# Performance work log

Measured on AMD Instinct MI355X. Metric: run time of the kernel, lower is better.

## Reference

```python
import jax, jax.numpy as jnp
import numpy as np

LAYERS = 2
HIDDEN = 512
FFN = 2048
HEADS = 8
IMG = (32, 64)
SLEN = IMG[0] * IMG[1]
BSZ = 2
KEY_DIM = HIDDEN // HEADS      # 64
V_DIM = HIDDEN * 2             # 1024
HEAD_SIZE = V_DIM // HEADS     # 128
SCALE_BASE = 512.0
SCALING = KEY_DIM ** (-0.5)
LN_EPS = 1e-5


def xpos_apply(x):
    # x: [..., L, d]  (XPOS rotary with length-dependent decay, downscale=False)
    L, d = x.shape[-2], x.shape[-1]
    half = d // 2
    base = (jnp.arange(0, d, 2, dtype=jnp.float32) + 0.4 * d) / (1.4 * d)  # [half]
    min_pos = -(L // 2)
    pos = jnp.arange(min_pos, L + min_pos, dtype=jnp.float32)              # [L]
    scale = base[None, :] ** (pos[:, None] / SCALE_BASE)                   # [L, half]
    inv_freq = 1.0 / (10000.0 ** (jnp.arange(half, dtype=jnp.float32) / half))
    sinusoid = jnp.arange(L, dtype=jnp.float32)[:, None] * inv_freq[None, :]  # [L, half]
    sin = jnp.repeat(jnp.sin(sinusoid) * scale, 2, axis=-1)                # [L, d]
    cos = jnp.repeat(jnp.cos(sinusoid) * scale, 2, axis=-1)                # [L, d]
    x1 = x[..., 0::2]
    x2 = x[..., 1::2]
    rot = jnp.stack([-x2, x1], axis=-1).reshape(x.shape)  # rotate_every_two
    return x * cos + rot * sin


def layer_norm(x, g, b):
    mu = jnp.mean(x, axis=-1, keepdims=True)
    var = jnp.mean(jnp.square(x - mu), axis=-1, keepdims=True)
    return (x - mu) * jax.lax.rsqrt(var + LN_EPS) * g + b


def attention(x, Wq, Wk, Wv, Wo):
    B, S, _ = x.shape
    q = (x @ Wq).reshape(B, S, HEADS, KEY_DIM).transpose(0, 2, 1, 3)   # [B,H,S,dk]
    k = (x @ Wk).reshape(B, S, HEADS, KEY_DIM).transpose(0, 2, 1, 3)
    v = (x @ Wv).reshape(B, S, HEADS, HEAD_SIZE).transpose(0, 2, 1, 3)  # [B,H,S,hs]
    q = xpos_apply(q)
    k = xpos_apply(k)
    scores = jnp.einsum('bhqd,bhkd->bhqk', q, k)
    att = jax.nn.softmax(scores.astype(jnp.float32), axis=-1).astype(scores.dtype)
    att = att * SCALING  # note: scaling applied AFTER softmax, as in the source
    out = jnp.einsum('bhqk,bhkv->bhqv', att, v)                          # [B,H,S,hs]
    out = out.transpose(0, 2, 1, 3).reshape(B, S, V_DIM)
    return out @ Wo


def setup_inputs() -> dict:
    key = jax.random.key(0)
    ks = jax.random.split(key, 8)
    p = lambda k, shp: jax.random.normal(k, shp, dtype=jnp.float32) * 0.02
    return {
        'x':  jax.random.normal(ks[0], (BSZ, SLEN, HIDDEN), dtype=jnp.float32),
        'Wq': p(ks[1], (LAYERS, HIDDEN, HIDDEN)),
        'Wk': p(ks[2], (LAYERS, HIDDEN, HIDDEN)),
        'Wv': p(ks[3], (LAYERS, HIDDEN, V_DIM)),
        'Wo': p(ks[4], (LAYERS, V_DIM, HIDDEN)),
        'W1': p(ks[5], (LAYERS, HIDDEN, FFN)),
        'b1': jnp.zeros((LAYERS, FFN), jnp.float32),
        'W2': p(ks[6], (LAYERS, FFN, HIDDEN)),
        'b2': jnp.zeros((LAYERS, HIDDEN), jnp.float32),
        'g1': jnp.ones((LAYERS, HIDDEN), jnp.float32),
        'be1': jnp.zeros((LAYERS, HIDDEN), jnp.float32),
        'g2': jnp.ones((LAYERS, HIDDEN), jnp.float32),
        'be2': jnp.zeros((LAYERS, HIDDEN), jnp.float32),
    }


def reference(x, Wq, Wk, Wv, Wo, W1, b1, W2, b2, g1, be1, g2, be2):
    for i in range(LAYERS):
        y = layer_norm(x + attention(x, Wq[i], Wk[i], Wv[i], Wo[i]), g1[i], be1[i])
        ffn = jax.nn.relu(y @ W1[i] + b1[i]) @ W2[i] + b2[i]
        x = layer_norm(y + ffn, g2[i], be2[i])
    return x.reshape(x.shape[0], IMG[0], IMG[1], x.shape[2])
```

## Files before the change

### kernel.cpp

```cpp
#include <hip/hip_runtime.h>
#include <hip/hip_bf16.h>
#include <math.h>

#define LAYERS 2
#define HIDDEN 512
#define FFN_DIM 2048
#define HEADS 8
#define SLEN 2048
#define BSZ 2
#define MROWS 4096
#define ATT_SCALING 0.125f
#define LN_EPS 1e-5f
#define SCALE_BASE 512.0f
#define LOG2E 1.4426950408889634f

typedef unsigned short u16;
typedef unsigned int u32;
typedef __attribute__((ext_vector_type(8))) short bf16x8;
typedef __attribute__((ext_vector_type(4))) float f32x4;

__device__ __forceinline__ float bf2f(u16 u) {
    union { u32 i; float f; } v; v.i = ((u32)u) << 16; return v.f;
}
__device__ __forceinline__ u16 f2bf(float f) {
    union { float f; u32 i; } v; v.f = f;
    u32 r = v.i + 0x7FFFu + ((v.i >> 16) & 1u);
    return (u16)(r >> 16);
}
__device__ __forceinline__ u32 pk2bf(float a, float b) {
    union { __hip_bfloat162 h; u32 u; } v;
    v.h = __float22bfloat162_rn(make_float2(a, b));
    return v.u;
}
__device__ __forceinline__ void async16(const void* g, void* l) {
    __builtin_amdgcn_global_load_lds((const __attribute__((address_space(1))) void*)g,
                                     (__attribute__((address_space(3))) void*)l, 16, 0, 0);
}

__global__ __launch_bounds__(256) void prep_kernel(const float* __restrict__ x,
                                                   const float* __restrict__ Wq,
                                                   const float* __restrict__ Wk,
                                                   const float* __restrict__ Wv,
                                                   const float* __restrict__ Wo,
                                                   const float* __restrict__ W1,
                                                   const float* __restrict__ W2,
                                                   char* __restrict__ w,
                                                   float* __restrict__ Af,
                                                   u16* __restrict__ Ab,
                                                   float2* __restrict__ tab) {
    const size_t MB1 = 1u << 20;
    const int bid = blockIdx.x;
    const int tid = threadIdx.x;
    __shared__ float t[32][33];

    if (bid < 7168) {
        int l = bid / 3584;
        int tt = bid % 3584;
        u16* WqkvT = (u16*)(w + 48 * MB1 + (size_t)l * 2 * MB1);
        u16* WoT   = (u16*)(w + 52 * MB1 + (size_t)l * 1 * MB1);
        u16* W1T   = (u16*)(w + 54 * MB1 + (size_t)l * 2 * MB1);
        u16* W2T   = (u16*)(w + 58 * MB1 + (size_t)l * 2 * MB1);
        const float* src; u16* dst; int K, N, tix;
        if (tt < 256)       { src = Wq + (size_t)l * 512 * 512;  dst = WqkvT;              K = 512;  N = 512;  tix = tt; }
        else if (tt < 512)  { src = Wk + (size_t)l * 512 * 512;  dst = WqkvT + 512 * 512;  K = 512;  N = 512;  tix = tt - 256; }
        else if (tt < 1024) { src = Wv + (size_t)l * 512 * 1024; dst = WqkvT + 1024 * 512; K = 512;  N = 1024; tix = tt - 512; }
        else if (tt < 1536) { src = Wo + (size_t)l * 1024 * 512; dst = WoT;                K = 1024; N = 512;  tix = tt - 1024; }
        else if (tt < 2560) { src = W1 + (size_t)l * 512 * 2048; dst = W1T;                K = 512;  N = 2048; tix = tt - 1536; }
        else                { src = W2 + (size_t)l * 2048 * 512; dst = W2T;                K = 2048; N = 512;  tix = tt - 2560; }
        int ntx = N >> 5;
        int n0 = (tix % ntx) * 32, k0 = (tix / ntx) * 32;
        int tx = tid & 31, ty = tid >> 5;
#pragma unroll
        for (int i = 0; i < 4; i++)
            t[ty + 8 * i][tx] = src[(size_t)(k0 + ty + 8 * i) * N + n0 + tx];
        __syncthreads();
#pragma unroll
        for (int i = 0; i < 4; i++)
            dst[(size_t)(n0 + ty + 8 * i) * K + k0 + tx] = f2bf(t[tx][ty + 8 * i]);
    } else if (bid < 9216) {
        int i = ((bid - 7168) * 256 + tid) * 4;
        float4 v = *(const float4*)(x + i);
        *(float4*)(Af + i) = v;
        uint2 p;
        p.x = pk2bf(v.x, v.y);
        p.y = pk2bf(v.z, v.w);
        *(uint2*)(Ab + i) = p;
    } else {
        int idx = (bid - 9216) * 256 + tid;
        int j = idx & 31;
        int s = idx >> 5;
        float base = (2.0f * j + 0.4f * 64.0f) / (1.4f * 64.0f);
        float pos = (float)(s - 1024);
        float scale = powf(base, pos / SCALE_BASE);
        float inv_freq = powf(10000.0f, -(float)j / 32.0f);
        float ang = (float)s * inv_freq;
        tab[idx] = make_float2(cosf(ang) * scale, sinf(ang) * scale);
    }
}

__global__ __launch_bounds__(256) void xpos_vtrans(u16* __restrict__ QKV,
                                                   const float2* __restrict__ tab,
                                                   u16* __restrict__ VT) {
    const int bid = blockIdx.x;
    const int tid = threadIdx.x;
    __shared__ u16 t[64][65];

    if (bid < 4096) {
        int idx = bid * 256 + tid;
        int j = idx & 31;
        int h = (idx >> 5) & 7;
        int s = (idx >> 8) & 2047;
        int b = idx >> 19;

        float2 cssn = tab[s * 32 + j];
        float cs = cssn.x, sn = cssn.y;

        size_t off = (size_t)(b * SLEN + s) * 2048 + h * 64 + 2 * j;
        u32* pq = (u32*)(QKV + off);
        u32* pk = (u32*)(QKV + off + 512);

        u32 qv = *pq;
        float q0 = bf2f((u16)(qv & 0xffff)), q1 = bf2f((u16)(qv >> 16));
        *pq = pk2bf((q0 * cs - q1 * sn) * LOG2E, (q1 * cs + q0 * sn) * LOG2E);

        u32 kv = *pk;
        float k0 = bf2f((u16)(kv & 0xffff)), k1 = bf2f((u16)(kv >> 16));
        *pk = pk2bf(k0 * cs - k1 * sn, k1 * cs + k0 * sn);
    } else {
        int v = bid - 4096;
        int bz = v & 15;
        int vy = (v >> 4) & 1;
        int sx = v >> 5;
        int b = bz >> 3, h = bz & 7;
        int s0 = sx * 64, v0 = vy * 64;
#pragma unroll
        for (int i = 0; i < 16; i++) {
            int e = tid + i * 256; int r = e >> 6, c = e & 63;
            t[r][c] = QKV[(size_t)(b * SLEN + s0 + r) * 2048 + 1024 + h * 128 + v0 + c];
        }
        __syncthreads();
#pragma unroll
        for (int i = 0; i < 16; i++) {
            int e = tid + i * 256; int r = e >> 6, c = e & 63;
            VT[(size_t)((b * 8 + h) * 128 + v0 + r) * 2048 + s0 + c] = t[c][r];
        }
    }
}

template <int BM, int BN, int BK, int WM, int OUTF32, int BIAS, int RELU, int NSPLIT>
__global__ __launch_bounds__(256) void gemm_mfma(const u16* __restrict__ A,
                                                 const u16* __restrict__ WT,
                                                 const float* __restrict__ bias,
                                                 void* __restrict__ C0,
                                                 void* __restrict__ C1,
                                                 int M, int N, int K) {
    constexpr int WN  = 4 / WM;
    constexpr int AM  = BM / (WM * 16);
    constexpr int AN  = BN / (WN * 16);
    constexpr int KO  = BK / 32;
    constexpr int AIT = BM * BK / 2048;
    constexpr int BIT = BN * BK / 2048;
    constexpr int KB8 = BK / 8;

    __shared__ u16 As[2][BM * BK];
    __shared__ u16 Bs[2][BN * BK];

    const int tid  = threadIdx.x;
    const int wave = tid >> 6;
    const int lane = tid & 63;
    const int quad = lane >> 4;
    const int l15  = lane & 15;
    const int wm = wave % WM;
    const int wn = wave / WM;

    const int tm = blockIdx.y * BM;
    const int tn = blockIdx.x * BN;
    const int z  = (NSPLIT > 1) ? blockIdx.z : 0;
    const int Ksub = K / NSPLIT;
    const int k0g  = z * Ksub;

    auto issue = [&](int kt, int buf) {
#pragma unroll
        for (int it = 0; it < AIT; it++) {
            int cid = it * 256 + tid;
            async16(A + (size_t)(tm + cid / KB8) * K + k0g + kt + (cid % KB8) * 8,
                    (char*)As[buf] + (it * 256 + wave * 64) * 16);
        }
#pragma unroll
        for (int it = 0; it < BIT; it++) {
            int cid = it * 256 + tid;
            async16(WT + (size_t)(tn + cid / KB8) * K + k0g + kt + (cid % KB8) * 8,
                    (char*)Bs[buf] + (it * 256 + wave * 64) * 16);
        }
    };

    f32x4 acc[AM][AN];
#pragma unroll
    for (int i = 0; i < AM; i++)
#pragma unroll
        for (int j = 0; j < AN; j++) acc[i][j] = (f32x4){0.f, 0.f, 0.f, 0.f};

    const int nk = Ksub / BK;
    issue(0, 0);

    for (int t = 0; t < nk; t++) {
        __syncthreads();
        if (t + 1 < nk) issue((t + 1) * BK, (t + 1) & 1);
        const int buf = t & 1;

        bf16x8 af[KO][AM], bfr[KO][AN];
#pragma unroll
        for (int ko = 0; ko < KO; ko++) {
#pragma unroll
            for (int i = 0; i < AM; i++)
                af[ko][i] = *(const bf16x8*)((const char*)As[buf] +
                    (((wm * (AM * 16) + i * 16 + l15) * KB8) + ko * 4 + quad) * 16);
#pragma unroll
            for (int j = 0; j < AN; j++)
                bfr[ko][j] = *(const bf16x8*)((const char*)Bs[buf] +
                    (((wn * (AN * 16) + j * 16 + l15) * KB8) + ko * 4 + quad) * 16);
        }
#pragma unroll
        for (int ko = 0; ko < KO; ko++)
#pragma unroll
            for (int i = 0; i < AM; i++)
#pragma unroll
                for (int j = 0; j < AN; j++)
                    acc[i][j] = __builtin_amdgcn_mfma_f32_16x16x32_bf16(
                        af[ko][i], bfr[ko][j], acc[i][j], 0, 0, 0);
    }

    void* Cout = (NSPLIT > 1 && z) ? C1 : C0;
#pragma unroll
    for (int i = 0; i < AM; i++) {
#pragma unroll
        for (int j = 0; j < AN; j++) {
            int col = tn + wn * (AN * 16) + j * 16 + l15;
            float bv = (BIAS && z == 0) ? bias[col] : 0.0f;
#pragma unroll
            for (int r = 0; r < 4; r++) {
                int row = tm + wm * (AM * 16) + i * 16 + quad * 4 + r;
                float v = acc[i][j][r] + bv;
                if (RELU) v = fmaxf(v, 0.0f);
                if (OUTF32) ((float*)Cout)[(size_t)row * N + col] = v;
                else        ((u16*)Cout)[(size_t)row * N + col] = f2bf(v);
            }
        }
    }
}

__global__ __launch_bounds__(256, 3) void flash_attn_mfma(const u16* __restrict__ QKV,
                                                          const u16* __restrict__ VT,
                                                          u16* __restrict__ OP0,
                                                          u16* __restrict__ OP1,
                                                          float2* __restrict__ ML) {
    const int h  = blockIdx.x;
    const int q0 = blockIdx.y * 64;
    const int bz = blockIdx.z;
    const int b  = bz >> 1;
    const int split = bz & 1;
    const int tid  = threadIdx.x;
    const int wave = tid >> 6;
    const int lane = tid & 63;
    const int quad = lane >> 4;
    const int l15  = lane & 15;
    const int swz  = quad ^ ((l15 >> 1) & 3);

    __shared__ u16 Ks[2][64 * 64];
    __shared__ u16 Vs[2][128 * 64];

    auto issueKV = [&](int kt, int buf) {
#pragma unroll
        for (int it = 0; it < 2; it++) {
            int cid = it * 256 + tid;
            int c = cid >> 8, p = cid & 255;
            async16(QKV + (size_t)(b * SLEN + kt + (p >> 2)) * 2048 + 512 + h * 64 +
                        c * 32 + (((p & 3) ^ ((p >> 3) & 3)) * 8),
                    (char*)Ks[buf] + (it * 256 + wave * 64) * 16);
        }
#pragma unroll
        for (int it = 0; it < 4; it++) {
            int cid = it * 256 + tid;
            int c = cid >> 9, p = cid & 511;
            async16(VT + (size_t)((b * 8 + h) * 128 + (p >> 2)) * 2048 + kt +
                        c * 32 + (((p & 3) ^ ((p >> 3) & 3)) * 8),
                    (char*)Vs[buf] + (it * 256 + wave * 64) * 16);
        }
    };

    bf16x8 qf[2];
    {
        const u16* p = QKV + (size_t)(b * SLEN + q0 + wave * 16 + l15) * 2048 +
                       h * 64 + quad * 8;
        qf[0] = *(const bf16x8*)p;
        qf[1] = *(const bf16x8*)(p + 32);
    }

    f32x4 o_acc[8];
#pragma unroll
    for (int t = 0; t < 8; t++) o_acc[t] = (f32x4){0.f, 0.f, 0.f, 0.f};
    float m = -1e30f;
    float l = 0.f;

    const int kb0 = split * 1024;
    issueKV(kb0, 0);

    for (int ti = 0; ti < 16; ti++) {
        __syncthreads();
        if (ti + 1 < 16) issueKV(kb0 + (ti + 1) * 64, (ti + 1) & 1);
        const int buf = ti & 1;

        f32x4 st[4];
#pragma unroll
        for (int t = 0; t < 4; t++) st[t] = (f32x4){0.f, 0.f, 0.f, 0.f};
        __builtin_amdgcn_s_setprio(1);
#pragma unroll
        for (int c = 0; c < 2; c++)
#pragma unroll
            for (int t = 0; t < 4; t++) {
                bf16x8 kb = *(const bf16x8*)((const char*)Ks[buf] + c * 4096 +
                             ((t * 16 + l15) * 4 + swz) * 16);
                st[t] = __builtin_amdgcn_mfma_f32_16x16x32_bf16(kb, qf[c],
                                                                st[t], 0, 0, 0);
            }
        __builtin_amdgcn_s_setprio(0);

        float mx = -1e30f;
#pragma unroll
        for (int t = 0; t < 4; t++)
#pragma unroll
            for (int r = 0; r < 4; r++) mx = fmaxf(mx, st[t][r]);
        mx = fmaxf(mx, __shfl_xor(mx, 16, 64));
        mx = fmaxf(mx, __shfl_xor(mx, 32, 64));

        float mnew = fmaxf(m, mx);
        float alpha = exp2f(m - mnew);
        float s = 0.f;
        u32 pp[4][2];
#pragma unroll
        for (int t = 0; t < 4; t++)
#pragma unroll
            for (int pr = 0; pr < 2; pr++) {
                float p0 = exp2f(st[t][2 * pr] - mnew);
                float p1 = exp2f(st[t][2 * pr + 1] - mnew);
                s += p0 + p1;
                pp[t][pr] = pk2bf(p0, p1);
            }
        m = mnew;
        s += __shfl_xor(s, 16, 64);
        s += __shfl_xor(s, 32, 64);
        l = l * alpha + s;

#pragma unroll
        for (int t = 0; t < 8; t++)
#pragma unroll
            for (int r = 0; r < 4; r++) o_acc[t][r] *= alpha;

#pragma unroll
        for (int c = 0; c < 2; c++) {
            union { u32 u[4]; bf16x8 v; } pu;
#pragma unroll
            for (int j2 = 0; j2 < 4; j2++) {
                int src = (2 * (quad & 1) + (j2 >> 1)) * 16 + l15;
                u32 g0 = (u32)__shfl((int)pp[2 * c][j2 & 1], src, 64);
                u32 g1 = (u32)__shfl((int)pp[2 * c + 1][j2 & 1], src, 64);
                pu.u[j2] = (quad & 2) ? g1 : g0;
            }
            __builtin_amdgcn_s_setprio(1);
#pragma unroll
            for (int t = 0; t < 8; t++) {
                bf16x8 vb = *(const bf16x8*)((const char*)Vs[buf] + c * 8192 +
                             ((t * 16 + l15) * 4 + swz) * 16);
                o_acc[t] = __builtin_amdgcn_mfma_f32_16x16x32_bf16(vb, pu.v,
                                                                   o_acc[t], 0, 0, 0);
            }
            __builtin_amdgcn_s_setprio(0);
        }
    }

    u16* OP = split ? OP1 : OP0;
    if (quad == 0)
        ML[((size_t)(split * 2 + b) * 8 + h) * 2048 + q0 + wave * 16 + l15] =
            make_float2(m, l);
    size_t rowbase = ((size_t)(b * SLEN + q0 + wave * 16 + l15)) * 1024 + h * 128;
#pragma unroll
    for (int t = 0; t < 8; t++)
#pragma unroll
        for (int rp = 0; rp < 2; rp++)
            *(u32*)(OP + rowbase + t * 16 + quad * 4 + 2 * rp) =
                pk2bf(o_acc[t][2 * rp], o_acc[t][2 * rp + 1]);
}

__global__ __launch_bounds__(256) void attn_combine(const u16* __restrict__ P0,
                                                    const u16* __restrict__ P1,
                                                    const float2* __restrict__ ML,
                                                    u16* __restrict__ AT) {
    int idx = (blockIdx.x * 256 + threadIdx.x) * 8;
    int hv = idx & 1023;
    int row = idx >> 10;
    int h = hv >> 7;
    int b = row >> 11, q = row & 2047;
    float2 ml0 = ML[((size_t)(0 + b) * 8 + h) * 2048 + q];
    float2 ml1 = ML[((size_t)(2 + b) * 8 + h) * 2048 + q];
    float M = fmaxf(ml0.x, ml1.x);
    float w0 = exp2f(ml0.x - M), w1 = exp2f(ml1.x - M);
    float L = ml0.y * w0 + ml1.y * w1;
    float sc = ATT_SCALING / L;
    w0 *= sc; w1 *= sc;

    uint4 a = *(const uint4*)(P0 + idx);
    uint4 c = *(const uint4*)(P1 + idx);
    uint4 o;
    u32 au[4] = {a.x, a.y, a.z, a.w};
    u32 cu[4] = {c.x, c.y, c.z, c.w};
    u32 ou[4];
#pragma unroll
    for (int k = 0; k < 4; k++) {
        float r0 = bf2f((u16)(au[k] & 0xffff)) * w0 + bf2f((u16)(cu[k] & 0xffff)) * w1;
        float r1 = bf2f((u16)(au[k] >> 16)) * w0 + bf2f((u16)(cu[k] >> 16)) * w1;
        ou[k] = pk2bf(r0, r1);
    }
    o.x = ou[0]; o.y = ou[1]; o.z = ou[2]; o.w = ou[3];
    *(uint4*)(AT + idx) = o;
}

__global__ __launch_bounds__(256) void addln_kernel(const float* __restrict__ X,
                                                    const float* __restrict__ R0,
                                                    const float* __restrict__ R1,
                                                    const float* __restrict__ g,
                                                    const float* __restrict__ be,
                                                    float* __restrict__ dstf,
                                                    u16* __restrict__ dstb) {
    const int row = blockIdx.x;
    const int tid = threadIdx.x;
    __shared__ float red[256];
    size_t off = (size_t)row * HIDDEN + 2 * tid;
    float2 a  = *(const float2*)(X + off);
    float2 r0 = *(const float2*)(R0 + off);
    float2 r1 = *(const float2*)(R1 + off);
    float v0 = a.x + r0.x + r1.x;
    float v1 = a.y + r0.y + r1.y;
    red[tid] = v0 + v1;
    __syncthreads();
    for (int s = 128; s > 0; s >>= 1) { if (tid < s) red[tid] += red[tid + s]; __syncthreads(); }
    float mu = red[0] * (1.0f / HIDDEN);
    __syncthreads();
    float d0 = v0 - mu, d1 = v1 - mu;
    red[tid] = d0 * d0 + d1 * d1;
    __syncthreads();
    for (int s = 128; s > 0; s >>= 1) { if (tid < s) red[tid] += red[tid + s]; __syncthreads(); }
    float rstd = rsqrtf(red[0] * (1.0f / HIDDEN) + LN_EPS);
    float2 gg = *(const float2*)(g + 2 * tid);
    float2 bb = *(const float2*)(be + 2 * tid);
    float o0 = d0 * rstd * gg.x + bb.x;
    float o1 = d1 * rstd * gg.y + bb.y;
    *(float2*)(dstf + off) = make_float2(o0, o1);
    *(u32*)(dstb + off) = pk2bf(o0, o1);
}

extern "C" void kernel_launch(void* const* d_in, const int* in_sizes, int n_in,
                              void* d_out, int out_size, void* d_ws, size_t ws_size,
                              hipStream_t stream) {
    const float* x   = (const float*)d_in[0];
    const float* Wq  = (const float*)d_in[1];
    const float* Wk  = (const float*)d_in[2];
    const float* Wv  = (const float*)d_in[3];
    const float* Wo  = (const float*)d_in[4];
    const float* W1  = (const float*)d_in[5];
    const float* b1  = (const float*)d_in[6];
    const float* W2  = (const float*)d_in[7];
    const float* b2  = (const float*)d_in[8];
    const float* g1  = (const float*)d_in[9];
    const float* be1 = (const float*)d_in[10];
    const float* g2  = (const float*)d_in[11];
    const float* be2 = (const float*)d_in[12];
    float* out = (float*)d_out;

    const size_t MB = 1u << 20;
    char* w = (char*)d_ws;
    float*  R1f  = (float*)(w);
    float*  F2a  = (float*)(w);
    u16*    VTg  = (u16*)(w + 8 * MB);
    float*  Yf   = (float*)(w + 8 * MB);
    u16*    OP1  = (u16*)(w + 16 * MB);
    float*  PfA  = (float*)(w + 16 * MB);
    float*  F2b  = (float*)(w + 16 * MB);
    u16*    QKV  = (u16*)(w + 24 * MB);
    float*  PfB  = (float*)(w + 24 * MB);
    u16*    F1   = (u16*)(w + 24 * MB);
    u16*    A_bf = (u16*)(w + 40 * MB);
    u16*    OP0  = (u16*)(w + 40 * MB);
    u16*    AT   = (u16*)(w + 40 * MB);
    u16*    Y_bf = (u16*)(w + 40 * MB);
    float2* xtab = (float2*)(w + 62 * MB);
    float2* ML   = (float2*)(w + 62 * MB + 512 * 1024);

    prep_kernel<<<9472, 256, 0, stream>>>(x, Wq, Wk, Wv, Wo, W1, W2,
                                          w, R1f, A_bf, xtab);

    for (int l = 0; l < LAYERS; l++) {
        u16* WqkvT = (u16*)(w + 48 * MB + (size_t)l * 2 * MB);
        u16* WoT   = (u16*)(w + 52 * MB + (size_t)l * 1 * MB);
        u16* W1T   = (u16*)(w + 54 * MB + (size_t)l * 2 * MB);
        u16* W2T   = (u16*)(w + 58 * MB + (size_t)l * 2 * MB);
        const float* b1_l  = b1 + (size_t)l * FFN_DIM;
        const float* b2_l  = b2 + (size_t)l * HIDDEN;
        const float* g1_l  = g1 + (size_t)l * HIDDEN;
        const float* be1_l = be1 + (size_t)l * HIDDEN;
        const float* g2_l  = g2 + (size_t)l * HIDDEN;
        const float* be2_l = be2 + (size_t)l * HIDDEN;

        gemm_mfma<128, 128, 64, 2, 0, 0, 0, 1><<<dim3(16, 32), 256, 0, stream>>>(
            A_bf, WqkvT, nullptr, QKV, nullptr, MROWS, 2048, 512);

        xpos_vtrans<<<5120, 256, 0, stream>>>(QKV, xtab, VTg);

        flash_attn_mfma<<<dim3(8, 32, 4), 256, 0, stream>>>(QKV, VTg, OP0, OP1, ML);
        attn_combine<<<MROWS * 1024 / 2048, 256, 0, stream>>>(OP0, OP1, ML, AT);

        gemm_mfma<128, 64, 64, 2, 1, 0, 0, 2><<<dim3(8, 32, 2), 256, 0, stream>>>(
            AT, WoT, nullptr, PfA, PfB, MROWS, 512, 1024);

        addln_kernel<<<MROWS, 256, 0, stream>>>(R1f, PfA, PfB, g1_l, be1_l, Yf, Y_bf);

        gemm_mfma<128, 128, 64, 2, 0, 1, 1, 1><<<dim3(16, 32), 256, 0, stream>>>(
            Y_bf, W1T, b1_l, F1, nullptr, MROWS, 2048, 512);

        gemm_mfma<128, 64, 64, 2, 1, 1, 0, 2><<<dim3(8, 32, 2), 256, 0, stream>>>(
            F1, W2T, b2_l, F2a, F2b, MROWS, 512, 2048);

        float* dstf = (l == LAYERS - 1) ? out : R1f;
        addln_kernel<<<MROWS, 256, 0, stream>>>(Yf, F2a, F2b, g2_l, be2_l, dstf, A_bf);
    }
}
```

Measured before the change: 432.4 us.

## Switch flash attention to 32x32x16 MFMA with 128-query tiles per block

Rewrites the flash attention kernel to use 32x32x16 bf16 MFMA instructions, with each wave owning 32 query rows, so a block covers 128 queries and the grid halves. The P-matrix relayout now uses v_permlane32_swap instead of several cross-lane shuffles, and the K/V LDS tiles get a new XOR swizzle matched to the 32-lane access pattern. The aim is to halve K/V reloads per query, cut shuffle overhead and raise MFMA efficiency. The cost is higher register pressure (occupancy hint lowered to 2) and fewer blocks to fill the GPU.

New measurement: 404.2 us. -6.5%, faster.

```diff
diff --git a/kernel.cpp b/kernel.cpp
--- a/kernel.cpp
+++ b/kernel.cpp
@@ -18,6 +18,7 @@
 typedef unsigned int u32;
 typedef __attribute__((ext_vector_type(8))) short bf16x8;
 typedef __attribute__((ext_vector_type(4))) float f32x4;
+typedef __attribute__((ext_vector_type(16))) float f32x16;
 
 __device__ __forceinline__ float bf2f(u16 u) {
     union { u32 i; float f; } v; v.i = ((u32)u) << 16; return v.f;
@@ -249,22 +250,22 @@
     }
 }
 
-__global__ __launch_bounds__(256, 3) void flash_attn_mfma(const u16* __restrict__ QKV,
+__global__ __launch_bounds__(256, 2) void flash_attn_mfma(const u16* __restrict__ QKV,
                                                           const u16* __restrict__ VT,
                                                           u16* __restrict__ OP0,
                                                           u16* __restrict__ OP1,
                                                           float2* __restrict__ ML) {
     const int h  = blockIdx.x;
-    const int q0 = blockIdx.y * 64;
+    const int q0 = blockIdx.y * 128;
     const int bz = blockIdx.z;
     const int b  = bz >> 1;
     const int split = bz & 1;
     const int tid  = threadIdx.x;
     const int wave = tid >> 6;
     const int lane = tid & 63;
-    const int quad = lane >> 4;
-    const int l15  = lane & 15;
-    const int swz  = quad ^ ((l15 >> 1) & 3);
+    const int l31  = lane & 31;
+    const int hi   = lane >> 5;
+    const int swz  = (l31 & 7) ^ ((l31 >> 3) << 1);
 
     __shared__ u16 Ks[2][64 * 64];
     __shared__ u16 Vs[2][128 * 64];
@@ -273,32 +274,34 @@
 #pragma unroll
         for (int it = 0; it < 2; it++) {
             int cid = it * 256 + tid;
-            int c = cid >> 8, p = cid & 255;
-            async16(QKV + (size_t)(b * SLEN + kt + (p >> 2)) * 2048 + 512 + h * 64 +
-                        c * 32 + (((p & 3) ^ ((p >> 3) & 3)) * 8),
+            int row = cid >> 3;
+            int lc  = (cid & 7) ^ (row & 7) ^ (((row >> 3) & 3) << 1);
+            async16(QKV + (size_t)(b * SLEN + kt + row) * 2048 + 512 + h * 64 + lc * 8,
                     (char*)Ks[buf] + (it * 256 + wave * 64) * 16);
         }
 #pragma unroll
         for (int it = 0; it < 4; it++) {
             int cid = it * 256 + tid;
-            int c = cid >> 9, p = cid & 511;
-            async16(VT + (size_t)((b * 8 + h) * 128 + (p >> 2)) * 2048 + kt +
-                        c * 32 + (((p & 3) ^ ((p >> 3) & 3)) * 8),
+            int row = cid >> 3;
+            int lc  = (cid & 7) ^ (row & 7) ^ (((row >> 3) & 3) << 1);
+            async16(VT + (size_t)((b * 8 + h) * 128 + row) * 2048 + kt + lc * 8,
                     (char*)Vs[buf] + (it * 256 + wave * 64) * 16);
         }
     };
 
-    bf16x8 qf[2];
+    bf16x8 qf[4];
     {
-        const u16* p = QKV + (size_t)(b * SLEN + q0 + wave * 16 + l15) * 2048 +
-                       h * 64 + quad * 8;
-        qf[0] = *(const bf16x8*)p;
-        qf[1] = *(const bf16x8*)(p + 32);
-    }
-
-    f32x4 o_acc[8];
-#pragma unroll
-    for (int t = 0; t < 8; t++) o_acc[t] = (f32x4){0.f, 0.f, 0.f, 0.f};
+        const u16* p = QKV + (size_t)(b * SLEN + q0 + wave * 32 + l31) * 2048 +
+                       h * 64 + hi * 8;
+#pragma unroll
+        for (int dc = 0; dc < 4; dc++) qf[dc] = *(const bf16x8*)(p + dc * 16);
+    }
+
+    f32x16 o_acc[4];
+#pragma unroll
+    for (int rb = 0; rb < 4; rb++)
+#pragma unroll
+        for (int r = 0; r < 16; r++) o_acc[rb][r] = 0.f;
     float m = -1e30f;
     float l = 0.f;
 
@@ -310,85 +313,86 @@
         if (ti + 1 < 16) issueKV(kb0 + (ti + 1) * 64, (ti + 1) & 1);
         const int buf = ti & 1;
 
-        f32x4 st[4];
-#pragma unroll
-        for (int t = 0; t < 4; t++) st[t] = (f32x4){0.f, 0.f, 0.f, 0.f};
+        f32x16 st[2];
+#pragma unroll
+        for (int kb = 0; kb < 2; kb++)
+#pragma unroll
+            for (int r = 0; r < 16; r++) st[kb][r] = 0.f;
         __builtin_amdgcn_s_setprio(1);
 #pragma unroll
-        for (int c = 0; c < 2; c++)
-#pragma unroll
-            for (int t = 0; t < 4; t++) {
-                bf16x8 kb = *(const bf16x8*)((const char*)Ks[buf] + c * 4096 +
-                             ((t * 16 + l15) * 4 + swz) * 16);
-                st[t] = __builtin_amdgcn_mfma_f32_16x16x32_bf16(kb, qf[c],
-                                                                st[t], 0, 0, 0);
+        for (int dc = 0; dc < 4; dc++)
+#pragma unroll
+            for (int kb = 0; kb < 2; kb++) {
+                bf16x8 kf = *(const bf16x8*)((const char*)Ks[buf] +
+                    ((kb * 32 + l31) * 8 + ((dc * 2 + hi) ^ swz)) * 16);
+                st[kb] = __builtin_amdgcn_mfma_f32_32x32x16_bf16(kf, qf[dc],
+                                                                 st[kb], 0, 0, 0);
             }
         __builtin_amdgcn_s_setprio(0);
 
         float mx = -1e30f;
 #pragma unroll
-        for (int t = 0; t < 4; t++)
-#pragma unroll
-            for (int r = 0; r < 4; r++) mx = fmaxf(mx, st[t][r]);
-        mx = fmaxf(mx, __shfl_xor(mx, 16, 64));
+        for (int kb = 0; kb < 2; kb++)
+#pragma unroll
+            for (int r = 0; r < 16; r++) mx = fmaxf(mx, st[kb][r]);
         mx = fmaxf(mx, __shfl_xor(mx, 32, 64));
 
         float mnew = fmaxf(m, mx);
         float alpha = exp2f(m - mnew);
-        float s = 0.f;
-        u32 pp[4][2];
-#pragma unroll
-        for (int t = 0; t < 4; t++)
-#pragma unroll
-            for (int pr = 0; pr < 2; pr++) {
-                float p0 = exp2f(st[t][2 * pr] - mnew);
-                float p1 = exp2f(st[t][2 * pr + 1] - mnew);
-                s += p0 + p1;
-                pp[t][pr] = pk2bf(p0, p1);
+        m = mnew;
+        float ls = 0.f;
+#pragma unroll
+        for (int kb = 0; kb < 2; kb++)
+#pragma unroll
+            for (int r = 0; r < 16; r++) {
+                float p = exp2f(st[kb][r] - mnew);
+                st[kb][r] = p;
+                ls += p;
             }
-        m = mnew;
-        s += __shfl_xor(s, 16, 64);
-        s += __shfl_xor(s, 32, 64);
-        l = l * alpha + s;
-
-#pragma unroll
-        for (int t = 0; t < 8; t++)
-#pragma unroll
-            for (int r = 0; r < 4; r++) o_acc[t][r] *= alpha;
-
-#pragma unroll
-        for (int c = 0; c < 2; c++) {
-            union { u32 u[4]; bf16x8 v; } pu;
-#pragma unroll
-            for (int j2 = 0; j2 < 4; j2++) {
-                int src = (2 * (quad & 1) + (j2 >> 1)) * 16 + l15;
-                u32 g0 = (u32)__shfl((int)pp[2 * c][j2 & 1], src, 64);
-                u32 g1 = (u32)__shfl((int)pp[2 * c + 1][j2 & 1], src, 64);
-                pu.u[j2] = (quad & 2) ? g1 : g0;
-            }
+        ls += __shfl_xor(ls, 32, 64);
+        l = l * alpha + ls;
+
+#pragma unroll
+        for (int rb = 0; rb < 4; rb++)
+#pragma unroll
+            for (int r = 0; r < 16; r++) o_acc[rb][r] *= alpha;
+
+#pragma unroll
+        for (int kc = 0; kc < 4; kc++) {
+            const int kb = kc >> 1, o = (kc & 1) * 8;
+            u32 a1 = pk2bf(st[kb][o + 0], st[kb][o + 1]);
+            u32 b1 = pk2bf(st[kb][o + 4], st[kb][o + 5]);
+            u32 a2 = pk2bf(st[kb][o + 2], st[kb][o + 3]);
+            u32 b2 = pk2bf(st[kb][o + 6], st[kb][o + 7]);
+            asm volatile("v_permlane32_swap_b32 %0, %1" : "+v"(a1), "+v"(b1));
+            asm volatile("v_permlane32_swap_b32 %0, %1" : "+v"(a2), "+v"(b2));
+            union { u32 u[4]; bf16x8 v; } pf;
+            pf.u[0] = a1; pf.u[1] = a2; pf.u[2] = b1; pf.u[3] = b2;
             __builtin_amdgcn_s_setprio(1);
 #pragma unroll
-            for (int t = 0; t < 8; t++) {
-                bf16x8 vb = *(const bf16x8*)((const char*)Vs[buf] + c * 8192 +
-                             ((t * 16 + l15) * 4 + swz) * 16);
-                o_acc[t] = __builtin_amdgcn_mfma_f32_16x16x32_bf16(vb, pu.v,
-                                                                   o_acc[t], 0, 0, 0);
+            for (int rb = 0; rb < 4; rb++) {
+                bf16x8 vb = *(const bf16x8*)((const char*)Vs[buf] +
+                    ((rb * 32 + l31) * 8 + ((kc * 2 + hi) ^ swz)) * 16);
+                o_acc[rb] = __builtin_amdgcn_mfma_f32_32x32x16_bf16(vb, pf.v,
+                                                                    o_acc[rb], 0, 0, 0);
             }
             __builtin_amdgcn_s_setprio(0);
         }
     }
 
     u16* OP = split ? OP1 : OP0;
-    if (quad == 0)
-        ML[((size_t)(split * 2 + b) * 8 + h) * 2048 + q0 + wave * 16 + l15] =
-            make_float2(m, l);
-    size_t rowbase = ((size_t)(b * SLEN + q0 + wave * 16 + l15)) * 1024 + h * 128;
-#pragma unroll
-    for (int t = 0; t < 8; t++)
-#pragma unroll
-        for (int rp = 0; rp < 2; rp++)
-            *(u32*)(OP + rowbase + t * 16 + quad * 4 + 2 * rp) =
-                pk2bf(o_acc[t][2 * rp], o_acc[t][2 * rp + 1]);
+    const int q = q0 + wave * 32 + l31;
+    if (lane < 32)
+        ML[((size_t)(split * 2 + b) * 8 + h) * 2048 + q] = make_float2(m, l);
+    size_t rowbase = ((size_t)(b * SLEN + q)) * 1024 + h * 128;
+#pragma unroll
+    for (int rb = 0; rb < 4; rb++)
+#pragma unroll
+        for (int i = 0; i < 8; i++) {
+            int v = rb * 32 + ((2 * i) & 3) + 8 * (i >> 1) + 4 * hi;
+            *(u32*)(OP + rowbase + v) =
+                pk2bf(o_acc[rb][2 * i], o_acc[rb][2 * i + 1]);
+        }
 }
 
 __global__ __launch_bounds__(256) void attn_combine(const u16* __restrict__ P0,
@@ -515,7 +519,7 @@
 
         xpos_vtrans<<<5120, 256, 0, stream>>>(QKV, xtab, VTg);
 
-        flash_attn_mfma<<<dim3(8, 32, 4), 256, 0, stream>>>(QKV, VTg, OP0, OP1, ML);
+        flash_attn_mfma<<<dim3(8, 16, 4), 256, 0, stream>>>(QKV, VTg, OP0, OP1, ML);
         attn_combine<<<MROWS * 1024 / 2048, 256, 0, stream>>>(OP0, OP1, ML, AT);
 
         gemm_mfma<128, 64, 64, 2, 1, 0, 0, 2><<<dim3(8, 32, 2), 256, 0, stream>>>(
```
